# Optimization experiments

Hardware: AMD Instinct MI355X
Metric: run time of the kernel (lower is better)

The kernel has to match this reference:

```python
import jax, jax.numpy as jnp
import numpy as np

B, N, D, H = 8, 1024, 512, 8
DK = D // H  # key_dim == val_dim == 64
LN_EPS = 1e-5


def setup_inputs() -> dict:
    key = jax.random.key(0)
    ks = jax.random.split(key, 16)
    stdv = 1.0 / np.sqrt(D)
    u = lambda k, shape, s: jax.random.uniform(k, shape, jnp.float32, -s, s)
    inp = {
        'q': jax.random.normal(ks[0], (B, N, D), jnp.float32),
        'mask': jax.random.uniform(ks[1], (B, N, N)) < 0.1,  # True = masked out
        # eps1 is torch.zeros in the source (never re-initialized); use small
        'eps1': jax.random.normal(ks[2], (D, D), jnp.float32) * 0.03,
        # 3 MLP layers, stacked on leading axis. Linear: y = x @ W.T + b
        'U_w': u(ks[3], (3, D, D), stdv), 'U_b': u(ks[4], (3, D), stdv),
        'V_w': u(ks[5], (3, D, D), stdv), 'V_b': u(ks[6], (3, D), stdv),
        'ln_g': jnp.ones((3, D), jnp.float32), 'ln_b': jnp.zeros((3, D), jnp.float32),
        'W_query': u(ks[7], (H, D, DK), 1.0 / np.sqrt(DK)),
        'W_key':   u(ks[8], (H, D, DK), 1.0 / np.sqrt(DK)),
        'W_val':   u(ks[9], (H, D, DK), 1.0 / np.sqrt(DK)),
        'W_out':   u(ks[10], (H, DK, D), stdv),
    }
    return inp


def _layer_norm(x, g, b):
    mu = jnp.mean(x, axis=-1, keepdims=True)
    var = jnp.mean(jnp.square(x - mu), axis=-1, keepdims=True)
    return (x - mu) * jax.lax.rsqrt(var + LN_EPS) * g + b


def _mlp_layer(x, Uw, Ub, Vw, Vb, g, b):
    # U1 -> (identity maxpool k=1) -> V1 -> LayerNorm -> ReLU -> residual
    y = x @ Uw.T + Ub
    y = y @ Vw.T + Vb
    y = _layer_norm(y, g, b)
    return x + jax.nn.relu(y)


def reference(q, mask, eps1, U_w, U_b, V_w, V_b, ln_g, ln_b,
              W_query, W_key, W_val, W_out):
    nf = 1.0 / np.sqrt(DK)  # norm_factor; applied to BOTH Q and K as in source
    h = q
    for l in range(3):
        h = _mlp_layer(h @ eps1, U_w[l], U_b[l], V_w[l], V_b[l], ln_g[l], ln_b[l])
    # per-head projections: (H,B,N,DK)
    Q = jnp.einsum('bqd,hdk->hbqk', q, W_query) * nf
    K = jnp.einsum('bgd,hdk->hbgk', h, W_key) * nf
    V = jnp.einsum('bgd,hdk->hbgk', h, W_val)
    scores = jnp.einsum('hbqk,hbgk->hbqg', Q, K)  # (H,B,N,N)
    scores = jnp.where(mask[None], -1e10, scores)
    attn = jax.nn.softmax(scores, axis=-1)
    heads = jnp.einsum('hbqg,hbgv->hbqv', attn, V)
    out = jnp.einsum('hbqv,hvd->bqd', heads, W_out)  # (B,N,D)
    return out
```

## Files before the change

### kernel.cpp

```cpp
#include <hip/hip_runtime.h>

typedef __attribute__((ext_vector_type(8))) short bhalf8;
typedef __attribute__((ext_vector_type(4))) short bhalf4;
typedef __attribute__((ext_vector_type(4))) float f32x4;

__device__ __forceinline__ ushort f2bf(float f) {
  unsigned u = __builtin_bit_cast(unsigned, f);
  unsigned r = u + 0x7fffu + ((u >> 16) & 1u);
  return (ushort)(r >> 16);
}

__device__ __forceinline__ void cvt8(const float* __restrict__ src, ushort* __restrict__ dst) {
  float4 a = *(const float4*)src, b = *(const float4*)(src + 4);
  ushort o[8] = {f2bf(a.x), f2bf(a.y), f2bf(a.z), f2bf(a.w),
                 f2bf(b.x), f2bf(b.y), f2bf(b.z), f2bf(b.w)};
  *(uint4*)dst = *(uint4*)o;
}

__device__ __forceinline__ void gld16(const ushort* g, ushort* l) {
  __builtin_amdgcn_global_load_lds((const __attribute__((address_space(1))) void*)g,
                                   (__attribute__((address_space(3))) void*)l, 16, 0, 0);
}

__global__ __launch_bounds__(256) void prep_kernel(
    const float* __restrict__ q, const int* __restrict__ mask,
    const float* __restrict__ eps1, const float* __restrict__ U_w,
    const float* __restrict__ V_w, const float* __restrict__ Wq,
    const float* __restrict__ Wk, const float* __restrict__ Wv,
    const float* __restrict__ Wo, const float* __restrict__ U_b,
    const float* __restrict__ V_b,
    ushort* __restrict__ qb, unsigned long long* __restrict__ minv,
    ushort* __restrict__ uwb, ushort* __restrict__ vwb,
    ushort* __restrict__ e1b, ushort* __restrict__ e1t,
    ushort* __restrict__ wqkv, ushort* __restrict__ wot,
    float* __restrict__ cvec) {
  int i = blockIdx.x * 256 + threadIdx.x;
  if (i < 524288) {
    cvt8(q + (size_t)i * 8, qb + (size_t)i * 8);
  } else if (i < 2621440) {
    int i2 = i - 524288;
    size_t j0 = (size_t)i2 * 4;
    int4 m = *(const int4*)(mask + j0);
    unsigned nib = (m.x == 0 ? 1u : 0u) | (m.y == 0 ? 2u : 0u) |
                   (m.z == 0 ? 4u : 0u) | (m.w == 0 ? 8u : 0u);
    unsigned long long part = (unsigned long long)nib << ((i2 & 15) * 4);
#pragma unroll
    for (int off = 1; off < 16; off <<= 1) part |= __shfl_xor(part, off, 16);
    if ((threadIdx.x & 15) == 0) {
      int b = (int)(j0 >> 20), qq = (int)((j0 >> 10) & 1023), g0 = (int)(j0 & 1023);
      minv[((size_t)b * 16 + (g0 >> 6)) * 1024 + qq] = part;
    }
  } else if (i < 2719744) {
    int j = (i - 2621440) * 8;
    cvt8(U_w + j, uwb + j);
  } else if (i < 2818048) {
    int j = (i - 2719744) * 8;
    cvt8(V_w + j, vwb + j);
  } else if (i < 2850816) {
    int j = (i - 2818048) * 8;
    cvt8(eps1 + j, e1b + j);
  } else if (i < 3112960) {
    int j = i - 2850816; int n = j >> 9, k = j & 511;
    e1t[j] = f2bf(eps1[k * 512 + n]);
  } else if (i < 3899392) {
    int j = i - 3112960; int n = j >> 9, d = j & 511;
    const float* W = (n < 512) ? Wq : (n < 1024 ? Wk : Wv);
    float sc = (n < 512) ? 0.02255252509f : 1.0f;
    int nl = n & 511;
    wqkv[j] = f2bf(W[((nl >> 6) * 512 + d) * 64 + (nl & 63)] * sc);
  } else if (i < 4161536) {
    int j = i - 3899392; int d = j >> 9, hv = j & 511;
    wot[j] = f2bf(Wo[hv * 512 + d]);
  } else {
    int j = i - 4161536;
    int idx = j >> 6, ln = j & 63;
    int l = idx >> 9;
    const float* vr = V_w + (size_t)idx * 512 + ln * 8;
    const float* ur = U_b + l * 512 + ln * 8;
    float s = 0;
#pragma unroll
    for (int t = 0; t < 8; t++) s += vr[t] * ur[t];
#pragma unroll
    for (int off = 1; off < 64; off <<= 1) s += __shfl_xor(s, off, 64);
    if (ln == 0) cvec[idx] = s + V_b[idx];
  }
}

template <int BN>
__global__ __launch_bounds__(256) void gemm_nt(
    const ushort* __restrict__ A0, const ushort* __restrict__ A1,
    const ushort* __restrict__ Bt0, const ushort* __restrict__ Bt1,
    int bsplit, int mstride, int M, int K,
    ushort* __restrict__ Oa, const float* __restrict__ ba, int ca,
    ushort* __restrict__ Ob, const float* __restrict__ bb2, int cb,
    ushort* __restrict__ Oc, const float* __restrict__ bc, int cc) {
  __shared__ ushort As[128 * 32];
  __shared__ ushort Bs[BN * 32];
  int tid = threadIdx.x;
  int wave = tid >> 6, lane = tid & 63;
  int quad = lane >> 4, col = lane & 15;
  int m0 = blockIdx.x * 128, n0 = blockIdx.y * BN;
  const ushort* A = (A1 && n0 >= 512) ? A1 : A0;
  const ushort* Bp = ((n0 < bsplit) ? Bt0 + (size_t)n0 * K
                                    : Bt1 + (size_t)(n0 - bsplit) * K) +
                     (size_t)(m0 >> 9) * mstride;
  constexpr int NI = BN / 32;
  int wm = (BN == 128) ? (wave >> 1) * 64 : (wave & 1) * 64;
  int wn = (BN == 128) ? (wave & 1) * 64 : (wave >> 1) * 32;
  f32x4 acc[4][NI] = {};
  int srow = wave * 16 + (lane >> 2);
  int skc = (lane & 3) * 8;
  const ushort* gA0 = A + (size_t)(m0 + srow) * K + skc;
  const ushort* gA1 = gA0 + (size_t)64 * K;
  const ushort* gB0 = Bp + (size_t)srow * K + skc;
  const ushort* gB1 = gB0 + (size_t)64 * K;
  ushort* lA0 = &As[wave * 16 * 32];
  ushort* lA1 = &As[(64 + wave * 16) * 32];
  ushort* lB0 = &Bs[wave * 16 * 32];
  ushort* lB1 = (BN == 128) ? &Bs[(64 + wave * 16) * 32] : nullptr;

  gld16(gA0, lA0);
  gld16(gA1, lA1);
  gld16(gB0, lB0);
  if (BN == 128) gld16(gB1, lB1);

  for (int k0 = 0; k0 < K; k0 += 32) {
    __syncthreads();
    bhalf8 af[4], bg[NI];
#pragma unroll
    for (int i = 0; i < 4; i++)
      af[i] = *(bhalf8*)&As[(wm + i * 16 + col) * 32 + quad * 8];
#pragma unroll
    for (int i = 0; i < NI; i++)
      bg[i] = *(bhalf8*)&Bs[(wn + i * 16 + col) * 32 + quad * 8];
    __syncthreads();
    if (k0 + 32 < K) {
      gld16(gA0 + k0 + 32, lA0);
      gld16(gA1 + k0 + 32, lA1);
      gld16(gB0 + k0 + 32, lB0);
      if (BN == 128) gld16(gB1 + k0 + 32, lB1);
    }
#pragma unroll
    for (int mi = 0; mi < 4; mi++)
#pragma unroll
      for (int ni = 0; ni < NI; ni++)
        acc[mi][ni] = __builtin_amdgcn_mfma_f32_16x16x32_bf16(af[mi], bg[ni], acc[mi][ni], 0, 0, 0);
  }

  int reg = n0 >> 9;
  ushort* O = (reg == 0) ? Oa : (reg == 1 ? Ob : Oc);
  const float* bs = (reg == 0) ? ba : (reg == 1 ? bb2 : bc);
  int code = (reg == 0) ? ca : (reg == 1 ? cb : cc);
#pragma unroll
  for (int mi = 0; mi < 4; mi++)
#pragma unroll
    for (int ni = 0; ni < NI; ni++) {
      int cn = n0 + wn + ni * 16 + col;
      int cnl = cn & 511;
      int cmb = m0 + wm + mi * 16 + quad * 4;
      float bv = bs ? bs[cnl] : 0.f;
      if (code == 2) {
        int bhh = (cmb >> 10) * 8 + (cnl >> 6);
        size_t base = ((size_t)bhh * 64 + ((cmb & 1023) >> 4)) * 1024 +
                      (size_t)((cnl >> 5) & 1) * 512 + (size_t)(cmb & 15) * 32 + (cnl & 31);
#pragma unroll
        for (int r = 0; r < 4; r++)
          O[base + r * 32] = f2bf(acc[mi][ni][r] + bv);
      } else if (code == 3) {
        int bhh = (cmb >> 10) * 8 + (cnl >> 6);
        int v = cnl & 63;
        size_t base = (size_t)bhh * 65536 + (size_t)((cmb & 1023) >> 4) * 1024 +
                      (size_t)(v >> 5) * 512 + (size_t)(v & 15) * 32 +
                      (size_t)(cmb & 15) * 2 + (size_t)((v >> 4) & 1) * 4;
        ushort4 pk;
        pk.x = f2bf(acc[mi][ni][0] + bv);
        pk.y = f2bf(acc[mi][ni][1] + bv);
        pk.z = f2bf(acc[mi][ni][2] + bv);
        pk.w = f2bf(acc[mi][ni][3] + bv);
        *(ushort4*)&O[base] = pk;
      } else if (code == 1) {
        float* Ff = (float*)O;
#pragma unroll
        for (int r = 0; r < 4; r++)
          Ff[(size_t)(cmb + r) * 512 + cnl] = acc[mi][ni][r] + bv;
      } else {
#pragma unroll
        for (int r = 0; r < 4; r++)
          O[(size_t)(cmb + r) * 512 + cnl] = f2bf(acc[mi][ni][r] + bv);
      }
    }
}

__global__ __launch_bounds__(256) void ln_kernel(
    const float* __restrict__ z, const ushort* __restrict__ tb,
    const float* __restrict__ lgam, const float* __restrict__ lbet,
    ushort* __restrict__ hb) {
  int row = blockIdx.x * 4 + (threadIdx.x >> 6);
  int lane = threadIdx.x & 63;
  int cbase = lane * 8;
  const float* zr = z + (size_t)row * 512 + cbase;
  float x[8];
  *(float4*)&x[0] = *(const float4*)zr;
  *(float4*)&x[4] = *(const float4*)(zr + 4);
  float sum = 0;
#pragma unroll
  for (int i = 0; i < 8; i++) sum += x[i];
#pragma unroll
  for (int off = 1; off < 64; off <<= 1) sum += __shfl_xor(sum, off, 64);
  float mu = sum * (1.f / 512.f);
  float vs = 0;
#pragma unroll
  for (int i = 0; i < 8; i++) { float d = x[i] - mu; vs += d * d; }
#pragma unroll
  for (int off = 1; off < 64; off <<= 1) vs += __shfl_xor(vs, off, 64);
  float rstd = rsqrtf(vs * (1.f / 512.f) + 1e-5f);
  uint4 tr = *(const uint4*)&tb[(size_t)row * 512 + cbase];
  float tv[8];
  {
    const unsigned* u = (const unsigned*)&tr;
#pragma unroll
    for (int w = 0; w < 4; w++) {
      tv[2 * w] = __builtin_bit_cast(float, u[w] << 16);
      tv[2 * w + 1] = __builtin_bit_cast(float, u[w] & 0xFFFF0000u);
    }
  }
  ushort outv[8];
#pragma unroll
  for (int i = 0; i < 8; i++) {
    float val = (x[i] - mu) * rstd * lgam[cbase + i] + lbet[cbase + i];
    outv[i] = f2bf(tv[i] + fmaxf(val, 0.f));
  }
  *(uint4*)&hb[(size_t)row * 512 + cbase] = *(uint4*)outv;
}

__global__ __launch_bounds__(256, 4) void attn_kernel(
    const ushort* __restrict__ QtT, const ushort* __restrict__ KtT,
    const ushort* __restrict__ VtT, const unsigned long long* __restrict__ minv,
    ushort* __restrict__ Op) {
  __shared__ ushort lds[16384];
  int bh = blockIdx.x;
  int b = bh >> 3, h = bh & 7;
  int tid = threadIdx.x, w = tid >> 6, lane = tid & 63;
  int quad = lane >> 4, col = lane & 15;
  int qt = blockIdx.y * 4 + w;
  const ushort* Kg = KtT + (size_t)bh * 65536 + tid * 8;
  const ushort* Vg = VtT + (size_t)bh * 65536 + tid * 8;
  const ushort* Qt = QtT + (size_t)bh * 65536 + col * 32 + quad * 8;
  bhalf8 bq0 = *(const bhalf8*)(Qt + (size_t)qt * 1024);
  bhalf8 bq1 = *(const bhalf8*)(Qt + (size_t)qt * 1024 + 512);
  f32x4 o[4] = {};
  float lsum = 0.f;
  const unsigned long long* mb = minv + (size_t)b * 16384 + qt * 16 + col;
  int kread = col * 32 + quad * 8;
  int vread = col * 32 + quad * 8;

  {
    ushort* lk = &lds[w * 512];
    ushort* lv = &lds[4096 + w * 512];
    gld16(Kg, lk); gld16(Kg + 2048, lk + 2048);
    gld16(Vg, lv); gld16(Vg + 2048, lv + 2048);
  }
  unsigned long long mcur = mb[0], mnxt = 0;

  for (int p = 0; p < 16; ++p) {
    int cb = (p & 1) * 8192;
    __syncthreads();
    bhalf8 ak[4][2];
    bhalf8 avp[4][2];
#pragma unroll
    for (int gt = 0; gt < 4; ++gt) {
      ak[gt][0] = *(const bhalf8*)&lds[cb + gt * 1024 + kread];
      ak[gt][1] = *(const bhalf8*)&lds[cb + gt * 1024 + 512 + kread];
      avp[gt][0] = *(const bhalf8*)&lds[cb + 4096 + gt * 1024 + vread];
      avp[gt][1] = *(const bhalf8*)&lds[cb + 4096 + gt * 1024 + 512 + vread];
    }
    __syncthreads();
    if (p < 15) {
      int nb = (cb ^ 8192);
      ushort* lk = &lds[nb + w * 512];
      ushort* lv = &lds[nb + 4096 + w * 512];
      const ushort* gk = Kg + (size_t)(p + 1) * 4096;
      const ushort* gv = Vg + (size_t)(p + 1) * 4096;
      gld16(gk, lk); gld16(gk + 2048, lk + 2048);
      gld16(gv, lv); gld16(gv + 2048, lv + 2048);
      mnxt = mb[(size_t)(p + 1) * 1024];
    }
#pragma unroll
    for (int gt = 0; gt < 4; ++gt) {
      f32x4 s = {};
      s = __builtin_amdgcn_mfma_f32_16x16x32_bf16(ak[gt][0], bq0, s, 0, 0, 0);
      s = __builtin_amdgcn_mfma_f32_16x16x32_bf16(ak[gt][1], bq1, s, 0, 0, 0);
      unsigned shq = (unsigned)(mcur >> (gt * 16 + quad * 4));
      unsigned pu[4];
#pragma unroll
      for (int r = 0; r < 4; ++r) {
        unsigned keep = (unsigned)((int)(shq << (31 - r)) >> 31);
        pu[r] = __builtin_bit_cast(unsigned, __builtin_amdgcn_exp2f(s[r])) & keep;
        lsum += __builtin_bit_cast(float, pu[r]);
      }
      uint2 pp;
      pp.x = ((pu[0] + 0x8000u) >> 16) | (((pu[1] + 0x8000u) >> 16) << 16);
      pp.y = ((pu[2] + 0x8000u) >> 16) | (((pu[3] + 0x8000u) >> 16) << 16);
      bhalf4 bp = __builtin_bit_cast(bhalf4, pp);
#pragma unroll
      for (int vt = 0; vt < 4; ++vt) {
        bhalf4 av = (vt & 1)
            ? __builtin_shufflevector(avp[gt][vt >> 1], avp[gt][vt >> 1], 4, 5, 6, 7)
            : __builtin_shufflevector(avp[gt][vt >> 1], avp[gt][vt >> 1], 0, 1, 2, 3);
        o[vt] = __builtin_amdgcn_mfma_f32_16x16x16bf16_1k(av, bp, o[vt], 0, 0, 0);
      }
    }
    mcur = mnxt;
  }

  lsum += __shfl_xor(lsum, 16, 64);
  lsum += __shfl_xor(lsum, 32, 64);
  float rl = __builtin_amdgcn_rcpf(lsum);
  int q = qt * 16 + col;
#pragma unroll
  for (int vt = 0; vt < 4; ++vt) {
    ushort4 pk;
    pk.x = f2bf(o[vt][0] * rl);
    pk.y = f2bf(o[vt][1] * rl);
    pk.z = f2bf(o[vt][2] * rl);
    pk.w = f2bf(o[vt][3] * rl);
    *(ushort4*)&Op[(size_t)(b * 1024 + q) * 512 + h * 64 + vt * 16 + quad * 4] = pk;
  }
}

extern "C" void kernel_launch(void* const* d_in, const int* in_sizes, int n_in,
                              void* d_out, int out_size, void* d_ws, size_t ws_size,
                              hipStream_t stream) {
  const float* q    = (const float*)d_in[0];
  const int*   mask = (const int*)d_in[1];
  const float* eps1 = (const float*)d_in[2];
  const float* U_w  = (const float*)d_in[3];
  const float* U_b  = (const float*)d_in[4];
  const float* V_w  = (const float*)d_in[5];
  const float* V_b  = (const float*)d_in[6];
  const float* ln_g = (const float*)d_in[7];
  const float* ln_b = (const float*)d_in[8];
  const float* Wq   = (const float*)d_in[9];
  const float* Wk   = (const float*)d_in[10];
  const float* Wv   = (const float*)d_in[11];
  const float* Wo   = (const float*)d_in[12];
  float* out = (float*)d_out;

  char* ws = (char*)d_ws;
  auto carve = [&](size_t bytes) { char* p = ws; ws += bytes; return p; };
  ushort* qb   = (ushort*)carve(8388608);
  ushort* uwb  = (ushort*)carve(1572864);
  ushort* vwb  = (ushort*)carve(1572864);
  ushort* e1b  = (ushort*)carve(524288);
  ushort* e1t  = (ushort*)carve(524288);
  ushort* wqkv = (ushort*)carve(1572864);
  ushort* wot  = (ushort*)carve(524288);
  ushort* A1b  = (ushort*)carve(1572864);
  ushort* Gtb  = (ushort*)carve(1572864);
  float*  cvec = (float*)carve(6144);
  unsigned long long* minv = (unsigned long long*)carve(1048576);
  ushort* tb   = (ushort*)carve(8388608);
  float*  zf   = (float*)carve(16777216);
  ushort* hb   = (ushort*)carve(8388608);
  ushort* Qtt  = (ushort*)carve(8388608);
  ushort* Ktt  = (ushort*)carve(8388608);
  ushort* Vtt  = (ushort*)carve(8388608);
  ushort* Ob   = (ushort*)carve(8388608);
  const int BIG = 1 << 30;

  prep_kernel<<<16640, 256, 0, stream>>>(q, mask, eps1, U_w, V_w, Wq, Wk, Wv, Wo,
                                         U_b, V_b, qb, minv, uwb, vwb, e1b, e1t,
                                         wqkv, wot, cvec);
  gemm_nt<128><<<dim3(4, 12), 256, 0, stream>>>(
      e1b, nullptr, uwb, nullptr, BIG, 0, 512, 512,
      A1b, nullptr, 0, A1b + 262144, nullptr, 0, A1b + 524288, nullptr, 0);
  gemm_nt<64><<<dim3(12, 8), 256, 0, stream>>>(
      vwb, nullptr, A1b, nullptr, BIG, 262144, 1536, 512,
      Gtb, nullptr, 0, nullptr, nullptr, 0, nullptr, nullptr, 0);
  const ushort* hsrc = qb;
  for (int l = 0; l < 3; l++) {
    gemm_nt<128><<<dim3(64, 8), 256, 0, stream>>>(
        hsrc, nullptr, e1t, Gtb + l * 262144, 512, 0, 8192, 512,
        tb, nullptr, 0, (ushort*)zf, cvec + l * 512, 1, nullptr, nullptr, 0);
    ln_kernel<<<2048, 256, 0, stream>>>(zf, tb, ln_g + l * 512, ln_b + l * 512, hb);
    hsrc = hb;
  }
  gemm_nt<128><<<dim3(64, 12), 256, 0, stream>>>(
      qb, hb, wqkv, nullptr, BIG, 0, 8192, 512,
      Qtt, nullptr, 2, Ktt, nullptr, 2, Vtt, nullptr, 3);
  attn_kernel<<<dim3(64, 16), 256, 0, stream>>>(Qtt, Ktt, Vtt, minv, Ob);
  gemm_nt<64><<<dim3(64, 8), 256, 0, stream>>>(
      Ob, nullptr, wot, nullptr, BIG, 0, 8192, 512,
      (ushort*)out, nullptr, 1, nullptr, nullptr, 0, nullptr, nullptr, 0);
}
```

Baseline: 283.6 us.

## Tile weight transposes through LDS and store pre-LayerNorm activations as bf16

The weight transposes in the prep kernel (eps1, QKV and output projection) now go through 64x64 tiles staged in shared memory. Each thread does coalesced vector loads and stores instead of strided scalar gathers, and the prep grid shrinks. The per-layer pre-LayerNorm activation z is also written as bf16 instead of fp32, which halves its write and read traffic between the GEMM and LayerNorm kernels. The cost is reduced precision in LayerNorm statistics, and a small cleanup merges the duplicate V read offset in the attention kernel.

```diff
diff --git a/kernel.cpp b/kernel.cpp
--- a/kernel.cpp
+++ b/kernel.cpp
@@ -20,6 +20,26 @@
 __device__ __forceinline__ void gld16(const ushort* g, ushort* l) {
   __builtin_amdgcn_global_load_lds((const __attribute__((address_space(1))) void*)g,
                                    (__attribute__((address_space(3))) void*)l, 16, 0, 0);
+}
+
+__device__ __forceinline__ void tile_tr64(const float* __restrict__ src, int ldsrc,
+                                          ushort* __restrict__ dst, int lddst,
+                                          float sc, ushort* tl, int tid) {
+  int r = tid >> 2, cg = (tid & 3) * 16;
+  const float* srow = src + (size_t)r * ldsrc + cg;
+  float4 a = *(const float4*)srow, b = *(const float4*)(srow + 4),
+         c = *(const float4*)(srow + 8), d = *(const float4*)(srow + 12);
+  float vals[16] = {a.x, a.y, a.z, a.w, b.x, b.y, b.z, b.w,
+                    c.x, c.y, c.z, c.w, d.x, d.y, d.z, d.w};
+#pragma unroll
+  for (int jj = 0; jj < 16; ++jj) tl[(cg + jj) * 66 + r] = f2bf(vals[jj] * sc);
+  __syncthreads();
+  int cc = tid >> 2, kg = (tid & 3) * 16;
+  uint4 w0 = *(const uint4*)&tl[cc * 66 + kg];
+  uint4 w1 = *(const uint4*)&tl[cc * 66 + kg + 8];
+  ushort* drow = dst + (size_t)cc * lddst + kg;
+  *(uint4*)drow = w0;
+  *(uint4*)(drow + 8) = w1;
 }
 
 __global__ __launch_bounds__(256) void prep_kernel(
@@ -34,11 +54,13 @@
     ushort* __restrict__ e1b, ushort* __restrict__ e1t,
     ushort* __restrict__ wqkv, ushort* __restrict__ wot,
     float* __restrict__ cvec) {
-  int i = blockIdx.x * 256 + threadIdx.x;
-  if (i < 524288) {
+  __shared__ ushort tl[64 * 66];
+  int bx = blockIdx.x, tid = threadIdx.x;
+  if (bx < 2048) {
+    int i = bx * 256 + tid;
     cvt8(q + (size_t)i * 8, qb + (size_t)i * 8);
-  } else if (i < 2621440) {
-    int i2 = i - 524288;
+  } else if (bx < 10240) {
+    int i2 = (bx - 2048) * 256 + tid;
     size_t j0 = (size_t)i2 * 4;
     int4 m = *(const int4*)(mask + j0);
     unsigned nib = (m.x == 0 ? 1u : 0u) | (m.y == 0 ? 2u : 0u) |
@@ -50,29 +72,34 @@
       int b = (int)(j0 >> 20), qq = (int)((j0 >> 10) & 1023), g0 = (int)(j0 & 1023);
       minv[((size_t)b * 16 + (g0 >> 6)) * 1024 + qq] = part;
     }
-  } else if (i < 2719744) {
-    int j = (i - 2621440) * 8;
+  } else if (bx < 10624) {
+    int j = ((bx - 10240) * 256 + tid) * 8;
     cvt8(U_w + j, uwb + j);
-  } else if (i < 2818048) {
-    int j = (i - 2719744) * 8;
+  } else if (bx < 11008) {
+    int j = ((bx - 10624) * 256 + tid) * 8;
     cvt8(V_w + j, vwb + j);
-  } else if (i < 2850816) {
-    int j = (i - 2818048) * 8;
+  } else if (bx < 11136) {
+    int j = ((bx - 11008) * 256 + tid) * 8;
     cvt8(eps1 + j, e1b + j);
-  } else if (i < 3112960) {
-    int j = i - 2850816; int n = j >> 9, k = j & 511;
-    e1t[j] = f2bf(eps1[k * 512 + n]);
-  } else if (i < 3899392) {
-    int j = i - 3112960; int n = j >> 9, d = j & 511;
-    const float* W = (n < 512) ? Wq : (n < 1024 ? Wk : Wv);
-    float sc = (n < 512) ? 0.02255252509f : 1.0f;
-    int nl = n & 511;
-    wqkv[j] = f2bf(W[((nl >> 6) * 512 + d) * 64 + (nl & 63)] * sc);
-  } else if (i < 4161536) {
-    int j = i - 3899392; int d = j >> 9, hv = j & 511;
-    wot[j] = f2bf(Wo[hv * 512 + d]);
+  } else if (bx < 11200) {
+    int b2 = bx - 11136;
+    int r0 = (b2 >> 3) * 64, c0 = (b2 & 7) * 64;
+    tile_tr64(eps1 + (size_t)r0 * 512 + c0, 512,
+              e1t + (size_t)c0 * 512 + r0, 512, 1.f, tl, tid);
+  } else if (bx < 11392) {
+    int b2 = bx - 11200;
+    int widx = b2 >> 6, h = (b2 >> 3) & 7, r0 = (b2 & 7) * 64;
+    const float* W = (widx == 0) ? Wq : (widx == 1 ? Wk : Wv);
+    float sc = (widx == 0) ? 0.02255252509f : 1.0f;
+    tile_tr64(W + ((size_t)h * 512 + r0) * 64, 64,
+              wqkv + ((size_t)widx * 512 + h * 64) * 512 + r0, 512, sc, tl, tid);
+  } else if (bx < 11456) {
+    int b2 = bx - 11392;
+    int r0 = (b2 >> 3) * 64, c0 = (b2 & 7) * 64;
+    tile_tr64(Wo + (size_t)r0 * 512 + c0, 512,
+              wot + (size_t)c0 * 512 + r0, 512, 1.f, tl, tid);
   } else {
-    int j = i - 4161536;
+    int j = (bx - 11456) * 256 + tid;
     int idx = j >> 6, ln = j & 63;
     int l = idx >> 9;
     const float* vr = V_w + (size_t)idx * 512 + ln * 8;
@@ -192,16 +219,22 @@
 }
 
 __global__ __launch_bounds__(256) void ln_kernel(
-    const float* __restrict__ z, const ushort* __restrict__ tb,
+    const ushort* __restrict__ z, const ushort* __restrict__ tb,
     const float* __restrict__ lgam, const float* __restrict__ lbet,
     ushort* __restrict__ hb) {
   int row = blockIdx.x * 4 + (threadIdx.x >> 6);
   int lane = threadIdx.x & 63;
   int cbase = lane * 8;
-  const float* zr = z + (size_t)row * 512 + cbase;
+  uint4 zr = *(const uint4*)&z[(size_t)row * 512 + cbase];
   float x[8];
-  *(float4*)&x[0] = *(const float4*)zr;
-  *(float4*)&x[4] = *(const float4*)(zr + 4);
+  {
+    const unsigned* u = (const unsigned*)&zr;
+#pragma unroll
+    for (int w = 0; w < 4; w++) {
+      x[2 * w] = __builtin_bit_cast(float, u[w] << 16);
+      x[2 * w + 1] = __builtin_bit_cast(float, u[w] & 0xFFFF0000u);
+    }
+  }
   float sum = 0;
 #pragma unroll
   for (int i = 0; i < 8; i++) sum += x[i];
@@ -252,7 +285,6 @@
   float lsum = 0.f;
   const unsigned long long* mb = minv + (size_t)b * 16384 + qt * 16 + col;
   int kread = col * 32 + quad * 8;
-  int vread = col * 32 + quad * 8;
 
   {
     ushort* lk = &lds[w * 512];
@@ -271,8 +303,8 @@
     for (int gt = 0; gt < 4; ++gt) {
       ak[gt][0] = *(const bhalf8*)&lds[cb + gt * 1024 + kread];
       ak[gt][1] = *(const bhalf8*)&lds[cb + gt * 1024 + 512 + kread];
-      avp[gt][0] = *(const bhalf8*)&lds[cb + 4096 + gt * 1024 + vread];
-      avp[gt][1] = *(const bhalf8*)&lds[cb + 4096 + gt * 1024 + 512 + vread];
+      avp[gt][0] = *(const bhalf8*)&lds[cb + 4096 + gt * 1024 + kread];
+      avp[gt][1] = *(const bhalf8*)&lds[cb + 4096 + gt * 1024 + 512 + kread];
     }
     __syncthreads();
     if (p < 15) {
@@ -360,7 +392,7 @@
   float*  cvec = (float*)carve(6144);
   unsigned long long* minv = (unsigned long long*)carve(1048576);
   ushort* tb   = (ushort*)carve(8388608);
-  float*  zf   = (float*)carve(16777216);
+  ushort* zb   = (ushort*)carve(8388608);
   ushort* hb   = (ushort*)carve(8388608);
   ushort* Qtt  = (ushort*)carve(8388608);
   ushort* Ktt  = (ushort*)carve(8388608);
@@ -368,7 +400,7 @@
   ushort* Ob   = (ushort*)carve(8388608);
   const int BIG = 1 << 30;
 
-  prep_kernel<<<16640, 256, 0, stream>>>(q, mask, eps1, U_w, V_w, Wq, Wk, Wv, Wo,
+  prep_kernel<<<11840, 256, 0, stream>>>(q, mask, eps1, U_w, V_w, Wq, Wk, Wv, Wo,
                                          U_b, V_b, qb, minv, uwb, vwb, e1b, e1t,
                                          wqkv, wot, cvec);
   gemm_nt<128><<<dim3(4, 12), 256, 0, stream>>>(
@@ -381,8 +413,8 @@
   for (int l = 0; l < 3; l++) {
     gemm_nt<128><<<dim3(64, 8), 256, 0, stream>>>(
         hsrc, nullptr, e1t, Gtb + l * 262144, 512, 0, 8192, 512,
-        tb, nullptr, 0, (ushort*)zf, cvec + l * 512, 1, nullptr, nullptr, 0);
-    ln_kernel<<<2048, 256, 0, stream>>>(zf, tb, ln_g + l * 512, ln_b + l * 512, hb);
+        tb, nullptr, 0, zb, cvec + l * 512, 0, nullptr, nullptr, 0);
+    ln_kernel<<<2048, 256, 0, stream>>>(zb, tb, ln_g + l * 512, ln_b + l * 512, hb);
     hsrc = hb;
   }
   gemm_nt<128><<<dim3(64, 12), 256, 0, stream>>>(
```

Result: faster. 277.4 us (-2.2%).
